# Performance work log

Measured on AMD Instinct MI355X. Metric: run time of the kernel, lower is better.

## Reference

```python
import jax, jax.numpy as jnp
import numpy as np

B, T, H, DIN, DOUT = 512, 256, 512, 514, 2
DT_OVER_TAU = 1.0 / 10.0

def retanh(a):
    return jnp.maximum(jnp.tanh(a), 0.0)

def setup_inputs() -> dict:
    key = jax.random.key(0)
    ks = jax.random.split(key, 5)
    x = jax.random.normal(ks[0], (B, T, DIN), dtype=jnp.float32)
    noise = jax.random.normal(ks[1], (B, T, H), dtype=jnp.float32) * 0.1
    W_x_ah = jax.random.normal(ks[2], (H, DIN), dtype=jnp.float32) / np.sqrt(DIN).astype(np.float32)
    b_ah = jnp.zeros((H,), dtype=jnp.float32)
    W_h_ah = jax.random.normal(ks[3], (H, H), dtype=jnp.float32) / np.sqrt(H).astype(np.float32)
    W_h_y = jnp.zeros((DOUT, H), dtype=jnp.float32)
    ah0 = jnp.zeros((H,), dtype=jnp.float32)
    return {"x": x, "noise": noise, "W_x_ah": W_x_ah, "b_ah": b_ah,
            "W_h_ah": W_h_ah, "W_h_y": W_h_y, "ah0": ah0}

def reference(x, noise, W_x_ah, b_ah, W_h_ah, W_h_y, ah0):
    batch = x.shape[0]
    # precompute input drive for all timesteps: [B,T,H]
    x2ah = jnp.einsum('btd,hd->bth', x, W_x_ah) + b_ah
    ah_init = jnp.broadcast_to(ah0, (batch, H))
    h_init = retanh(ah_init)

    def step(carry, inp):
        ah, h = carry
        xt, nt = inp  # [B,H], [B,H]
        ah = ah + DT_OVER_TAU * (-ah + h @ W_h_ah.T + xt)
        h = retanh(ah) + nt
        return (ah, h), h

    xs = (jnp.swapaxes(x2ah, 0, 1), jnp.swapaxes(noise, 0, 1))  # [T,B,H]
    _, hs = jax.lax.scan(step, (ah_init, h_init), xs)
    hstore = jnp.swapaxes(hs, 0, 1)  # [B,T,H]
    output = jnp.einsum('bth,oh->bto', hstore, W_h_y)
    return output, hstore
```

## Files before the change

### kernel.cpp

```cpp
#include <hip/hip_runtime.h>
#include <math.h>

#define BB   512
#define TT   256
#define HH   512
#define DIN  514
#define DOUTN 2
#define DT   0.1f
#define TH   (TT * HH)

#define NSL   4
#define NGRP  32

typedef short s16x8 __attribute__((ext_vector_type(8)));
typedef float f32x4 __attribute__((ext_vector_type(4)));

__device__ __forceinline__ float retanh_f(float a) {
    float am = fminf(a, 15.0f);
    float E  = __expf(2.0f * am);
    float tp = __fdividef(E - 1.0f, E + 1.0f);
    return a > 0.0f ? tp : 0.0f;
}

__device__ __forceinline__ unsigned short f2bf(float f) {
    unsigned u = __float_as_uint(f);
    unsigned r = (u + 0x7FFFu + ((u >> 16) & 1u)) >> 16;
    return (unsigned short)r;
}

__device__ __forceinline__ void gload_lds16(const void* g, void* l) {
    __builtin_amdgcn_global_load_lds(
        (const __attribute__((address_space(1))) unsigned int*)g,
        (__attribute__((address_space(3))) unsigned int*)l, 16, 0, 0);
}

__global__ __launch_bounds__(256) void pack_wh(const float* __restrict__ Wh,
                                               unsigned short* __restrict__ Wp) {
    const int idx = blockIdx.x * 256 + threadIdx.x;
    const int l  = idx & 63;
    const int jt = (idx >> 6) & 31;
    const int kc = idx >> 11;
    const int j  = jt * 16 + (l & 15);
    const int k0 = kc * 32 + (l >> 4) * 8;
    s16x8 pv;
    #pragma unroll
    for (int e = 0; e < 8; ++e) pv[e] = (short)f2bf(Wh[j * HH + k0 + e]);
    *(s16x8*)&Wp[(size_t)idx * 8] = pv;
}

__global__ __launch_bounds__(256) void pack_wx(const float* __restrict__ Wx,
                                               unsigned short* __restrict__ WfH,
                                               unsigned short* __restrict__ WfL) {
    const int idx = blockIdx.x * 256 + threadIdx.x;
    const int l  = idx & 63;
    const int jt = (idx >> 6) & 31;
    const int kc = idx >> 11;
    const int j  = jt * 16 + (l & 15);
    const int k0 = kc * 32 + (l >> 4) * 8;
    s16x8 ph, pl;
    #pragma unroll
    for (int e = 0; e < 8; ++e) {
        const float v = Wx[(size_t)j * DIN + k0 + e];
        const unsigned short hi = f2bf(v);
        const float hv = __uint_as_float((unsigned)hi << 16);
        ph[e] = (short)hi;
        pl[e] = (short)f2bf(v - hv);
    }
    *(s16x8*)&WfH[(size_t)idx * 8] = ph;
    *(s16x8*)&WfL[(size_t)idx * 8] = pl;
}

__device__ __forceinline__ void cvt_hilo(float4 a, float4 b, s16x8& hi, s16x8& lo) {
    float v[8] = {a.x, a.y, a.z, a.w, b.x, b.y, b.z, b.w};
    #pragma unroll
    for (int e = 0; e < 8; ++e) {
        const unsigned short h = f2bf(v[e]);
        hi[e] = (short)h;
        lo[e] = (short)f2bf(v[e] - __uint_as_float((unsigned)h << 16));
    }
}

#define STAGE_W(KC, DST) do { \
    const s16x8* gh = WfHv + (size_t)(KC) * 2048 + w * 256 + l; \
    const s16x8* gl = WfLv + (size_t)(KC) * 2048 + w * 256 + l; \
    s16x8* dh = (DST) + w * 256; \
    s16x8* dl = (DST) + 2048 + w * 256; \
    gload_lds16(gh + 0 * 64, dh + 0 * 64); \
    gload_lds16(gh + 1 * 64, dh + 1 * 64); \
    gload_lds16(gh + 2 * 64, dh + 2 * 64); \
    gload_lds16(gh + 3 * 64, dh + 3 * 64); \
    gload_lds16(gl + 0 * 64, dl + 0 * 64); \
    gload_lds16(gl + 1 * 64, dl + 1 * 64); \
    gload_lds16(gl + 2 * 64, dl + 2 * 64); \
    gload_lds16(gl + 3 * 64, dl + 3 * 64); \
} while (0)

__global__ __launch_bounds__(512) void x2ah_mfma(const float* __restrict__ X,
                                                 const unsigned short* __restrict__ WfH,
                                                 const unsigned short* __restrict__ WfL,
                                                 const float* __restrict__ Wx,
                                                 const float* __restrict__ bias,
                                                 const float* __restrict__ noise,
                                                 unsigned int* __restrict__ outp) {
    __shared__ __align__(16) char arena[2][65536];

    const int tid = threadIdx.x;
    const int l   = tid & 63;
    const int w   = tid >> 6;
    const int lm  = l & 15;
    const int lg  = l >> 4;
    const int lg4 = lg * 4;
    const int lg8 = lg * 8;
    const int r0  = blockIdx.x * 128;

    const int rt  = w & 3;
    const int jt0 = (w >> 2) * 16;

    const s16x8* WfHv = (const s16x8*)WfH;
    const s16x8* WfLv = (const s16x8*)WfL;

    const float* xr0 = X + (size_t)(r0 + rt * 32 + lm) * DIN;
    const float* xr1 = xr0 + 16 * DIN;

    float4 xa0 = *(const float4*)(xr0 + lg8);
    float4 xb0 = *(const float4*)(xr0 + lg8 + 4);
    float4 xa1 = *(const float4*)(xr1 + lg8);
    float4 xb1 = *(const float4*)(xr1 + lg8 + 4);
    STAGE_W(0, (s16x8*)arena[0]);
    __syncthreads();

    f32x4 acc0[16], acc1[16];
    #pragma unroll
    for (int jt = 0; jt < 16; ++jt) {
        acc0[jt] = (f32x4){0.f, 0.f, 0.f, 0.f};
        acc1[jt] = (f32x4){0.f, 0.f, 0.f, 0.f};
    }

    for (int kc = 0; kc < 16; ++kc) {
        s16x8* cur = (s16x8*)arena[kc & 1];
        s16x8* nxt = (s16x8*)arena[(kc & 1) ^ 1];
        if (kc < 15) STAGE_W(kc + 1, nxt);

        s16x8 Ah0, Al0, Ah1, Al1;
        cvt_hilo(xa0, xb0, Ah0, Al0);
        cvt_hilo(xa1, xb1, Ah1, Al1);
        if (kc < 15) {
            const int off = (kc + 1) * 32 + lg8;
            xa0 = *(const float4*)(xr0 + off);
            xb0 = *(const float4*)(xr0 + off + 4);
            xa1 = *(const float4*)(xr1 + off);
            xb1 = *(const float4*)(xr1 + off + 4);
        }

        #pragma unroll
        for (int jt = 0; jt < 16; ++jt) {
            const s16x8 Bh = cur[(jt0 + jt) * 64 + l];
            const s16x8 Bl = cur[2048 + (jt0 + jt) * 64 + l];
            acc0[jt] = __builtin_amdgcn_mfma_f32_16x16x32_bf16(Ah0, Bh, acc0[jt], 0, 0, 0);
            acc0[jt] = __builtin_amdgcn_mfma_f32_16x16x32_bf16(Al0, Bh, acc0[jt], 0, 0, 0);
            acc0[jt] = __builtin_amdgcn_mfma_f32_16x16x32_bf16(Ah0, Bl, acc0[jt], 0, 0, 0);
            acc1[jt] = __builtin_amdgcn_mfma_f32_16x16x32_bf16(Ah1, Bh, acc1[jt], 0, 0, 0);
            acc1[jt] = __builtin_amdgcn_mfma_f32_16x16x32_bf16(Al1, Bh, acc1[jt], 0, 0, 0);
            acc1[jt] = __builtin_amdgcn_mfma_f32_16x16x32_bf16(Ah1, Bl, acc1[jt], 0, 0, 0);
        }
        __syncthreads();
    }

    unsigned short* ls = (unsigned short*)arena;
    for (int c = 0; c < 8; ++c) {
        if (rt == (c >> 1)) {
            float xt0[4], xt1[4];
            #pragma unroll
            for (int r = 0; r < 4; ++r) {
                const float* xrow = X + (size_t)(r0 + c * 16 + lg4 + r) * DIN + 512;
                xt0[r] = xrow[0];
                xt1[r] = xrow[1];
            }
            #pragma unroll
            for (int jt = 0; jt < 16; ++jt) {
                const int j = (jt0 + jt) * 16 + lm;
                const float2 wt = *(const float2*)&Wx[(size_t)j * DIN + 512];
                const float bj = bias[j];
                #pragma unroll
                for (int r = 0; r < 4; ++r) {
                    const float av = (c & 1) ? acc1[jt][r] : acc0[jt][r];
                    const float v = av + bj + xt0[r] * wt.x + xt1[r] * wt.y;
                    ls[(lg4 + r) * 512 + j] = f2bf(v);
                }
            }
        }
        __syncthreads();
        {
            const int i   = tid * 16;
            const int row = i >> 9, col = i & 511;
            const size_t gi = (size_t)(r0 + c * 16 + row) * HH + col;
            const float4 n0 = *(const float4*)&noise[gi + 0];
            const float4 n1 = *(const float4*)&noise[gi + 4];
            const float4 n2 = *(const float4*)&noise[gi + 8];
            const float4 n3 = *(const float4*)&noise[gi + 12];
            const unsigned short* lp = &ls[row * 512 + col];
            const uint4 la = *(const uint4*)lp;
            const uint4 lb = *(const uint4*)(lp + 8);
            uint4 o0, o1, o2, o3;
            o0.x = ((la.x & 0xffffu) << 16) | f2bf(n0.x);
            o0.y = (la.x & 0xffff0000u)     | f2bf(n0.y);
            o0.z = ((la.y & 0xffffu) << 16) | f2bf(n0.z);
            o0.w = (la.y & 0xffff0000u)     | f2bf(n0.w);
            o1.x = ((la.z & 0xffffu) << 16) | f2bf(n1.x);
            o1.y = (la.z & 0xffff0000u)     | f2bf(n1.y);
            o1.z = ((la.w & 0xffffu) << 16) | f2bf(n1.z);
            o1.w = (la.w & 0xffff0000u)     | f2bf(n1.w);
            o2.x = ((lb.x & 0xffffu) << 16) | f2bf(n2.x);
            o2.y = (lb.x & 0xffff0000u)     | f2bf(n2.y);
            o2.z = ((lb.y & 0xffffu) << 16) | f2bf(n2.z);
            o2.w = (lb.y & 0xffff0000u)     | f2bf(n2.w);
            o3.x = ((lb.z & 0xffffu) << 16) | f2bf(n3.x);
            o3.y = (lb.z & 0xffff0000u)     | f2bf(n3.y);
            o3.z = ((lb.w & 0xffffu) << 16) | f2bf(n3.z);
            o3.w = (lb.w & 0xffff0000u)     | f2bf(n3.w);
            *(uint4*)&outp[gi + 0]  = o0;
            *(uint4*)&outp[gi + 4]  = o1;
            *(uint4*)&outp[gi + 8]  = o2;
            *(uint4*)&outp[gi + 12] = o3;
        }
        __syncthreads();
    }
}

#define WKLOAD(KC) s16x8 wk##KC = WpV[((KC) * 32 + s * 8 + w) * 64 + l]
#define WKPIN(A, B, C, D) asm volatile("" : "+v"(A), "+v"(B), "+v"(C), "+v"(D))

#define KC_EVEN(KC) do { \
    const s16x8 A = *(const s16x8*)&hrow[(KC) * 32]; \
    accA = __builtin_amdgcn_mfma_f32_16x16x32_bf16(A, wk##KC, accA, 0, 0, 0); \
} while (0)
#define KC_ODD(KC) do { \
    const s16x8 A = *(const s16x8*)&hrow[(KC) * 32]; \
    accB = __builtin_amdgcn_mfma_f32_16x16x32_bf16(A, wk##KC, accB, 0, 0, 0); \
} while (0)

__global__ __launch_bounds__(512) void scan12_kernel(const unsigned short* __restrict__ Wp,
                                                     const float* __restrict__ ah0,
                                                     unsigned int* __restrict__ hio,
                                                     unsigned short* inbox,
                                                     unsigned int* flags) {
    __shared__ __align__(16) unsigned short hs[16][520];

    const int tid = threadIdx.x;
    const int l   = tid & 63;
    const int w   = tid >> 6;
    const int lm  = l & 15;
    const int lg  = l >> 4;
    const int lg4 = lg * 4;
    const int gid = blockIdx.x;
    const int g   = gid >> 2;
    const int s   = gid & 3;
    const int b0  = g * 16;

    const s16x8* WpV = (const s16x8*)Wp;

    WKLOAD(0);  WKLOAD(1);  WKLOAD(2);  WKLOAD(3);
    WKLOAD(4);  WKLOAD(5);  WKLOAD(6);  WKLOAD(7);
    WKLOAD(8);  WKLOAD(9);  WKLOAD(10); WKLOAD(11);
    WKLOAD(12); WKLOAD(13); WKLOAD(14); WKLOAD(15);
    WKPIN(wk0, wk1, wk2, wk3);     WKPIN(wk4, wk5, wk6, wk7);
    WKPIN(wk8, wk9, wk10, wk11);   WKPIN(wk12, wk13, wk14, wk15);

    const int jn = (s * 8 + w) * 16 + lm;

    f32x4 ahv;
    {
        const float a0 = ah0[jn];
        ahv = (f32x4){a0, a0, a0, a0};
    }

    for (int idx = tid; idx < 16 * 512; idx += 512) {
        int b = idx >> 9, k = idx & 511;
        hs[b][k] = f2bf(retanh_f(ah0[k]));
    }
    __syncthreads();

    const unsigned short* hrow = &hs[lm][lg * 8];

    const int pb = tid >> 5;
    const int pq = tid & 31;
    unsigned long long* ibx = (unsigned long long*)inbox;
    const int pubIdx = (((b0 + pb) << 9) + s * 128 + pq * 4) >> 2;
    const int gatIdx = ((b0 + pb) << 7) + pq;

    int gb = (b0 + lg4) * TH + jn;

    unsigned int pk0 = hio[gb + 0 * TH];
    unsigned int pk1 = hio[gb + 1 * TH];
    unsigned int pk2 = hio[gb + 2 * TH];
    unsigned int pk3 = hio[gb + 3 * TH];

    for (int t = 0; t < TT; ++t) {
        const int par = (t & 1) << 16;

        f32x4 accA = (f32x4){0.f, 0.f, 0.f, 0.f};
        f32x4 accB = (f32x4){0.f, 0.f, 0.f, 0.f};
        KC_EVEN(0);  KC_ODD(1);  KC_EVEN(2);  KC_ODD(3);
        KC_EVEN(4);  KC_ODD(5);  KC_EVEN(6);  KC_ODD(7);
        KC_EVEN(8);  KC_ODD(9);  KC_EVEN(10); KC_ODD(11);
        KC_EVEN(12); KC_ODD(13); KC_EVEN(14); KC_ODD(15);
        const f32x4 acc = accA + accB;

        __syncthreads();

        {
            float a, h;
            unsigned int p;
            p = pk0; a = ahv[0];
            a += DT * (acc[0] + __uint_as_float(p & 0xffff0000u) - a);
            ahv[0] = a; h = retanh_f(a) + __uint_as_float(p << 16);
            hio[gb + 0 * TH] = __float_as_uint(h); hs[lg4 + 0][jn] = f2bf(h);
            p = pk1; a = ahv[1];
            a += DT * (acc[1] + __uint_as_float(p & 0xffff0000u) - a);
            ahv[1] = a; h = retanh_f(a) + __uint_as_float(p << 16);
            hio[gb + 1 * TH] = __float_as_uint(h); hs[lg4 + 1][jn] = f2bf(h);
            p = pk2; a = ahv[2];
            a += DT * (acc[2] + __uint_as_float(p & 0xffff0000u) - a);
            ahv[2] = a; h = retanh_f(a) + __uint_as_float(p << 16);
            hio[gb + 2 * TH] = __float_as_uint(h); hs[lg4 + 2][jn] = f2bf(h);
            p = pk3; a = ahv[3];
            a += DT * (acc[3] + __uint_as_float(p & 0xffff0000u) - a);
            ahv[3] = a; h = retanh_f(a) + __uint_as_float(p << 16);
            hio[gb + 3 * TH] = __float_as_uint(h); hs[lg4 + 3][jn] = f2bf(h);
        }

        __syncthreads();

        {
            const unsigned long long pub =
                *(const unsigned long long*)&hs[pb][s * 128 + pq * 4];
            __hip_atomic_store(&ibx[par + pubIdx], pub, __ATOMIC_RELAXED,
                               __HIP_MEMORY_SCOPE_AGENT);
        }
        asm volatile("s_waitcnt vmcnt(0)" ::: "memory");
        __syncthreads();

        unsigned int* fl = flags + (t * NGRP + g) * NSL;
        if (tid == 0)
            __hip_atomic_store(&fl[s], 1u, __ATOMIC_RELAXED, __HIP_MEMORY_SCOPE_AGENT);

        if (t + 1 < TT) {
            pk0 = hio[gb + HH + 0 * TH];
            pk1 = hio[gb + HH + 1 * TH];
            pk2 = hio[gb + HH + 2 * TH];
            pk3 = hio[gb + HH + 3 * TH];
        }

        if (tid < NSL) {
            while (__hip_atomic_load(&fl[tid], __ATOMIC_RELAXED,
                                     __HIP_MEMORY_SCOPE_AGENT) == 0u)
                __builtin_amdgcn_s_sleep(1);
        }
        __syncthreads();

        {
            const unsigned long long g0 = __hip_atomic_load(&ibx[par + gatIdx + 0 * 32],
                __ATOMIC_RELAXED, __HIP_MEMORY_SCOPE_AGENT);
            const unsigned long long g1 = __hip_atomic_load(&ibx[par + gatIdx + 1 * 32],
                __ATOMIC_RELAXED, __HIP_MEMORY_SCOPE_AGENT);
            const unsigned long long g2 = __hip_atomic_load(&ibx[par + gatIdx + 2 * 32],
                __ATOMIC_RELAXED, __HIP_MEMORY_SCOPE_AGENT);
            const unsigned long long g3 = __hip_atomic_load(&ibx[par + gatIdx + 3 * 32],
                __ATOMIC_RELAXED, __HIP_MEMORY_SCOPE_AGENT);
            *(unsigned long long*)&hs[pb][pq * 4 + 0 * 128] = g0;
            *(unsigned long long*)&hs[pb][pq * 4 + 1 * 128] = g1;
            *(unsigned long long*)&hs[pb][pq * 4 + 2 * 128] = g2;
            *(unsigned long long*)&hs[pb][pq * 4 + 3 * 128] = g3;
        }
        __syncthreads();

        gb += HH;
    }
}

__global__ __launch_bounds__(256) void out_kernel(const float* __restrict__ hstore,
                                                  const float* __restrict__ Wy,
                                                  float* __restrict__ out0) {
    const int wave = threadIdx.x >> 6;
    const int lane = threadIdx.x & 63;
    const int r = blockIdx.x * 4 + wave;

    const float4* hv4 = (const float4*)&hstore[r * HH];
    float a0 = 0.0f, a1 = 0.0f;
    #pragma unroll
    for (int u = 0; u < 2; ++u) {
        const int e = u * 64 + lane;
        const float4 h  = hv4[e];
        const float4 w0 = *(const float4*)&Wy[e * 4];
        const float4 w1 = *(const float4*)&Wy[HH + e * 4];
        a0 += h.x * w0.x + h.y * w0.y + h.z * w0.z + h.w * w0.w;
        a1 += h.x * w1.x + h.y * w1.y + h.z * w1.z + h.w * w1.w;
    }
    #pragma unroll
    for (int off = 32; off > 0; off >>= 1) {
        a0 += __shfl_xor(a0, off);
        a1 += __shfl_xor(a1, off);
    }
    if (lane == 0) {
        out0[r * 2]     = a0;
        out0[r * 2 + 1] = a1;
    }
}

extern "C" void kernel_launch(void* const* d_in, const int* in_sizes, int n_in,
                              void* d_out, int out_size, void* d_ws, size_t ws_size,
                              hipStream_t stream) {
    const float* x     = (const float*)d_in[0];
    const float* noise = (const float*)d_in[1];
    const float* Wx    = (const float*)d_in[2];
    const float* bah   = (const float*)d_in[3];
    const float* Wh    = (const float*)d_in[4];
    const float* Wy    = (const float*)d_in[5];
    const float* ah0   = (const float*)d_in[6];

    float* out0   = (float*)d_out;
    float* hstore = (float*)d_out + BB * TT * DOUTN;

    const size_t FRAG_U16 = (size_t)16 * 32 * 64 * 8;
    unsigned short* Wp    = (unsigned short*)d_ws;
    unsigned short* WxH   = Wp + FRAG_U16;
    unsigned short* WxL   = WxH + FRAG_U16;
    unsigned short* inbox = WxL + FRAG_U16;
    unsigned int*   flags = (unsigned int*)(inbox + 2 * BB * HH);

    pack_wh<<<16 * 32 * 64 / 256, 256, 0, stream>>>(Wh, Wp);
    pack_wx<<<16 * 32 * 64 / 256, 256, 0, stream>>>(Wx, WxH, WxL);
    x2ah_mfma<<<BB * TT / 128, 512, 0, stream>>>(x, WxH, WxL, Wx, bah, noise,
                                                 (unsigned int*)hstore);

    hipMemsetAsync(flags, 0, (size_t)TT * NGRP * NSL * sizeof(unsigned int), stream);
    {
        const unsigned short* wpp = Wp;
        unsigned int* hiop = (unsigned int*)hstore;
        unsigned short* ibp = inbox;
        unsigned int* flp = flags;
        void* args[] = { (void*)&wpp, (void*)&ah0, (void*)&hiop,
                         (void*)&ibp, (void*)&flp };
        hipLaunchCooperativeKernel((void*)scan12_kernel, dim3(NGRP * NSL),
                                   dim3(512), args, 0, stream);
    }

    out_kernel<<<BB * TT / 4, 256, 0, stream>>>(hstore, Wy, out0);
}
```

Before: 1.119 ms.

## Publish per-wave h directly to inbox with per-wave flags and fuse output projection

Each wave now writes its bf16 h values straight to the global inbox and raises its own flag, so two block-wide barriers and the shared-memory staging step before publishing are gone. Consumers spin on 32 per-wave flags instead of 4 per-block flags. The hstore writes move after the flag store, off the critical path. The separate output-projection kernel is folded into the scan using gathered bf16 h, which removes a pass over hstore but computes the output from bf16 rather than fp32 h.

New measurement: 1.192 ms. +6.5%, slower.

```diff
diff --git a/kernel.cpp b/kernel.cpp
--- a/kernel.cpp
+++ b/kernel.cpp
@@ -239,12 +239,15 @@
     accB = __builtin_amdgcn_mfma_f32_16x16x32_bf16(A, wk##KC, accB, 0, 0, 0); \
 } while (0)
 
-__global__ __launch_bounds__(512) void scan12_kernel(const unsigned short* __restrict__ Wp,
+__global__ __launch_bounds__(512) void scan15_kernel(const unsigned short* __restrict__ Wp,
                                                      const float* __restrict__ ah0,
+                                                     const float* __restrict__ Wy,
                                                      unsigned int* __restrict__ hio,
+                                                     float* __restrict__ out0,
                                                      unsigned short* inbox,
                                                      unsigned int* flags) {
     __shared__ __align__(16) unsigned short hs[16][520];
+    __shared__ float wy[2][512];
 
     const int tid = threadIdx.x;
     const int l   = tid & 63;
@@ -274,6 +277,7 @@
         ahv = (f32x4){a0, a0, a0, a0};
     }
 
+    for (int i = tid; i < 2 * 512; i += 512) wy[i >> 9][i & 511] = Wy[i];
     for (int idx = tid; idx < 16 * 512; idx += 512) {
         int b = idx >> 9, k = idx & 511;
         hs[b][k] = f2bf(retanh_f(ah0[k]));
@@ -285,8 +289,11 @@
     const int pb = tid >> 5;
     const int pq = tid & 31;
     unsigned long long* ibx = (unsigned long long*)inbox;
-    const int pubIdx = (((b0 + pb) << 9) + s * 128 + pq * 4) >> 2;
     const int gatIdx = ((b0 + pb) << 7) + pq;
+    const int pubBase = (b0 + lg4) * 512 + jn;
+
+    const int obid = 4 * s + (w >> 1);
+    const int oo   = w & 1;
 
     int gb = (b0 + lg4) * TH + jn;
 
@@ -296,7 +303,8 @@
     unsigned int pk3 = hio[gb + 3 * TH];
 
     for (int t = 0; t < TT; ++t) {
-        const int par = (t & 1) << 16;
+        const int par64 = (t & 1) << 16;
+        const int par16 = (t & 1) << 18;
 
         f32x4 accA = (f32x4){0.f, 0.f, 0.f, 0.f};
         f32x4 accB = (f32x4){0.f, 0.f, 0.f, 0.f};
@@ -306,44 +314,44 @@
         KC_EVEN(12); KC_ODD(13); KC_EVEN(14); KC_ODD(15);
         const f32x4 acc = accA + accB;
 
-        __syncthreads();
-
+        float h0f, h1f, h2f, h3f;
         {
-            float a, h;
-            unsigned int p;
-            p = pk0; a = ahv[0];
-            a += DT * (acc[0] + __uint_as_float(p & 0xffff0000u) - a);
-            ahv[0] = a; h = retanh_f(a) + __uint_as_float(p << 16);
-            hio[gb + 0 * TH] = __float_as_uint(h); hs[lg4 + 0][jn] = f2bf(h);
-            p = pk1; a = ahv[1];
-            a += DT * (acc[1] + __uint_as_float(p & 0xffff0000u) - a);
-            ahv[1] = a; h = retanh_f(a) + __uint_as_float(p << 16);
-            hio[gb + 1 * TH] = __float_as_uint(h); hs[lg4 + 1][jn] = f2bf(h);
-            p = pk2; a = ahv[2];
-            a += DT * (acc[2] + __uint_as_float(p & 0xffff0000u) - a);
-            ahv[2] = a; h = retanh_f(a) + __uint_as_float(p << 16);
-            hio[gb + 2 * TH] = __float_as_uint(h); hs[lg4 + 2][jn] = f2bf(h);
-            p = pk3; a = ahv[3];
-            a += DT * (acc[3] + __uint_as_float(p & 0xffff0000u) - a);
-            ahv[3] = a; h = retanh_f(a) + __uint_as_float(p << 16);
-            hio[gb + 3 * TH] = __float_as_uint(h); hs[lg4 + 3][jn] = f2bf(h);
-        }
-
-        __syncthreads();
+            float a;
+            a = ahv[0];
+            a += DT * (acc[0] + __uint_as_float(pk0 & 0xffff0000u) - a);
+            ahv[0] = a; h0f = retanh_f(a) + __uint_as_float(pk0 << 16);
+            a = ahv[1];
+            a += DT * (acc[1] + __uint_as_float(pk1 & 0xffff0000u) - a);
+            ahv[1] = a; h1f = retanh_f(a) + __uint_as_float(pk1 << 16);
+            a = ahv[2];
+            a += DT * (acc[2] + __uint_as_float(pk2 & 0xffff0000u) - a);
+            ahv[2] = a; h2f = retanh_f(a) + __uint_as_float(pk2 << 16);
+            a = ahv[3];
+            a += DT * (acc[3] + __uint_as_float(pk3 & 0xffff0000u) - a);
+            ahv[3] = a; h3f = retanh_f(a) + __uint_as_float(pk3 << 16);
+        }
 
         {
-            const unsigned long long pub =
-                *(const unsigned long long*)&hs[pb][s * 128 + pq * 4];
-            __hip_atomic_store(&ibx[par + pubIdx], pub, __ATOMIC_RELAXED,
+            unsigned short* pbase = inbox + par16 + pubBase;
+            __hip_atomic_store(&pbase[0 * 512], f2bf(h0f), __ATOMIC_RELAXED,
                                __HIP_MEMORY_SCOPE_AGENT);
+            __hip_atomic_store(&pbase[1 * 512], f2bf(h1f), __ATOMIC_RELAXED,
+                               __HIP_MEMORY_SCOPE_AGENT);
+            __hip_atomic_store(&pbase[2 * 512], f2bf(h2f), __ATOMIC_RELAXED,
+                               __HIP_MEMORY_SCOPE_AGENT);
+            __hip_atomic_store(&pbase[3 * 512], f2bf(h3f), __ATOMIC_RELAXED,
+                               __HIP_MEMORY_SCOPE_AGENT);
         }
         asm volatile("s_waitcnt vmcnt(0)" ::: "memory");
-        __syncthreads();
-
-        unsigned int* fl = flags + (t * NGRP + g) * NSL;
-        if (tid == 0)
-            __hip_atomic_store(&fl[s], 1u, __ATOMIC_RELAXED, __HIP_MEMORY_SCOPE_AGENT);
-
+
+        unsigned int* fl = flags + ((size_t)(t * NGRP + g) * NSL + s) * 8;
+        if (l == 0)
+            __hip_atomic_store(&fl[w], 1u, __ATOMIC_RELAXED, __HIP_MEMORY_SCOPE_AGENT);
+
+        hio[gb + 0 * TH] = __float_as_uint(h0f);
+        hio[gb + 1 * TH] = __float_as_uint(h1f);
+        hio[gb + 2 * TH] = __float_as_uint(h2f);
+        hio[gb + 3 * TH] = __float_as_uint(h3f);
         if (t + 1 < TT) {
             pk0 = hio[gb + HH + 0 * TH];
             pk1 = hio[gb + HH + 1 * TH];
@@ -351,21 +359,23 @@
             pk3 = hio[gb + HH + 3 * TH];
         }
 
-        if (tid < NSL) {
-            while (__hip_atomic_load(&fl[tid], __ATOMIC_RELAXED,
+        if (tid < 32) {
+            const unsigned int* fp = flags
+                + ((size_t)(t * NGRP + g) * NSL + (tid >> 3)) * 8 + (tid & 7);
+            while (__hip_atomic_load(fp, __ATOMIC_RELAXED,
                                      __HIP_MEMORY_SCOPE_AGENT) == 0u)
                 __builtin_amdgcn_s_sleep(1);
         }
         __syncthreads();
 
         {
-            const unsigned long long g0 = __hip_atomic_load(&ibx[par + gatIdx + 0 * 32],
+            const unsigned long long g0 = __hip_atomic_load(&ibx[par64 + gatIdx + 0 * 32],
                 __ATOMIC_RELAXED, __HIP_MEMORY_SCOPE_AGENT);
-            const unsigned long long g1 = __hip_atomic_load(&ibx[par + gatIdx + 1 * 32],
+            const unsigned long long g1 = __hip_atomic_load(&ibx[par64 + gatIdx + 1 * 32],
                 __ATOMIC_RELAXED, __HIP_MEMORY_SCOPE_AGENT);
-            const unsigned long long g2 = __hip_atomic_load(&ibx[par + gatIdx + 2 * 32],
+            const unsigned long long g2 = __hip_atomic_load(&ibx[par64 + gatIdx + 2 * 32],
                 __ATOMIC_RELAXED, __HIP_MEMORY_SCOPE_AGENT);
-            const unsigned long long g3 = __hip_atomic_load(&ibx[par + gatIdx + 3 * 32],
+            const unsigned long long g3 = __hip_atomic_load(&ibx[par64 + gatIdx + 3 * 32],
                 __ATOMIC_RELAXED, __HIP_MEMORY_SCOPE_AGENT);
             *(unsigned long long*)&hs[pb][pq * 4 + 0 * 128] = g0;
             *(unsigned long long*)&hs[pb][pq * 4 + 1 * 128] = g1;
@@ -374,36 +384,25 @@
         }
         __syncthreads();
 
+        {
+            const s16x8 hv = *(const s16x8*)&hs[obid][l * 8];
+            const float4 w0 = *(const float4*)&wy[oo][l * 8];
+            const float4 w1 = *(const float4*)&wy[oo][l * 8 + 4];
+            float p = __uint_as_float(((unsigned)(unsigned short)hv[0]) << 16) * w0.x
+                    + __uint_as_float(((unsigned)(unsigned short)hv[1]) << 16) * w0.y
+                    + __uint_as_float(((unsigned)(unsigned short)hv[2]) << 16) * w0.z
+                    + __uint_as_float(((unsigned)(unsigned short)hv[3]) << 16) * w0.w
+                    + __uint_as_float(((unsigned)(unsigned short)hv[4]) << 16) * w1.x
+                    + __uint_as_float(((unsigned)(unsigned short)hv[5]) << 16) * w1.y
+                    + __uint_as_float(((unsigned)(unsigned short)hv[6]) << 16) * w1.z
+                    + __uint_as_float(((unsigned)(unsigned short)hv[7]) << 16) * w1.w;
+            #pragma unroll
+            for (int off = 32; off > 0; off >>= 1) p += __shfl_xor(p, off);
+            if (l == 0)
+                out0[((size_t)(b0 + obid) * TT + t) * 2 + oo] = p;
+        }
+
         gb += HH;
-    }
-}
-
-__global__ __launch_bounds__(256) void out_kernel(const float* __restrict__ hstore,
-                                                  const float* __restrict__ Wy,
-                                                  float* __restrict__ out0) {
-    const int wave = threadIdx.x >> 6;
-    const int lane = threadIdx.x & 63;
-    const int r = blockIdx.x * 4 + wave;
-
-    const float4* hv4 = (const float4*)&hstore[r * HH];
-    float a0 = 0.0f, a1 = 0.0f;
-    #pragma unroll
-    for (int u = 0; u < 2; ++u) {
-        const int e = u * 64 + lane;
-        const float4 h  = hv4[e];
-        const float4 w0 = *(const float4*)&Wy[e * 4];
-        const float4 w1 = *(const float4*)&Wy[HH + e * 4];
-        a0 += h.x * w0.x + h.y * w0.y + h.z * w0.z + h.w * w0.w;
-        a1 += h.x * w1.x + h.y * w1.y + h.z * w1.z + h.w * w1.w;
-    }
-    #pragma unroll
-    for (int off = 32; off > 0; off >>= 1) {
-        a0 += __shfl_xor(a0, off);
-        a1 += __shfl_xor(a1, off);
-    }
-    if (lane == 0) {
-        out0[r * 2]     = a0;
-        out0[r * 2 + 1] = a1;
     }
 }
 
@@ -433,17 +432,17 @@
     x2ah_mfma<<<BB * TT / 128, 512, 0, stream>>>(x, WxH, WxL, Wx, bah, noise,
                                                  (unsigned int*)hstore);
 
-    hipMemsetAsync(flags, 0, (size_t)TT * NGRP * NSL * sizeof(unsigned int), stream);
+    hipMemsetAsync(flags, 0, (size_t)TT * NGRP * NSL * 8 * sizeof(unsigned int),
+                   stream);
     {
         const unsigned short* wpp = Wp;
         unsigned int* hiop = (unsigned int*)hstore;
+        float* outp = out0;
         unsigned short* ibp = inbox;
         unsigned int* flp = flags;
-        void* args[] = { (void*)&wpp, (void*)&ah0, (void*)&hiop,
-                         (void*)&ibp, (void*)&flp };
-        hipLaunchCooperativeKernel((void*)scan12_kernel, dim3(NGRP * NSL),
+        void* args[] = { (void*)&wpp, (void*)&ah0, (void*)&Wy, (void*)&hiop,
+                         (void*)&outp, (void*)&ibp, (void*)&flp };
+        hipLaunchCooperativeKernel((void*)scan15_kernel, dim3(NGRP * NSL),
                                    dim3(512), args, 0, stream);
     }
-
-    out_kernel<<<BB * TT / 4, 256, 0, stream>>>(hstore, Wy, out0);
-}
+}
```

## Interleave two batch groups per block to hide cross-block flag waits

Applied to the files above, without the earlier changes.

Each block now owns two 16-row batch groups and alternates them within a timestep. While it waits for one group's slices from the other blocks, it computes the recurrent GEMM and update for the other group, so the cross-block exchange latency overlaps useful work. The global hstore writes are also moved after the inbox publish and flag store, taking them off the critical path. The grid is halved to 64 blocks, so fewer CUs are active and each block carries twice the serial work per step.

New measurement: 1.705 ms. 1.52x slower.

```diff
diff --git a/kernel.cpp b/kernel.cpp
--- a/kernel.cpp
+++ b/kernel.cpp
@@ -230,21 +230,31 @@
 #define WKLOAD(KC) s16x8 wk##KC = WpV[((KC) * 32 + s * 8 + w) * 64 + l]
 #define WKPIN(A, B, C, D) asm volatile("" : "+v"(A), "+v"(B), "+v"(C), "+v"(D))
 
-#define KC_EVEN(KC) do { \
-    const s16x8 A = *(const s16x8*)&hrow[(KC) * 32]; \
+#define KC_EVEN(HR, KC) do { \
+    const s16x8 A = *(const s16x8*)&(HR)[(KC) * 32]; \
     accA = __builtin_amdgcn_mfma_f32_16x16x32_bf16(A, wk##KC, accA, 0, 0, 0); \
 } while (0)
-#define KC_ODD(KC) do { \
-    const s16x8 A = *(const s16x8*)&hrow[(KC) * 32]; \
+#define KC_ODD(HR, KC) do { \
+    const s16x8 A = *(const s16x8*)&(HR)[(KC) * 32]; \
     accB = __builtin_amdgcn_mfma_f32_16x16x32_bf16(A, wk##KC, accB, 0, 0, 0); \
 } while (0)
 
-__global__ __launch_bounds__(512) void scan12_kernel(const unsigned short* __restrict__ Wp,
+#define GEMM16(HR, ACC) do { \
+    f32x4 accA = (f32x4){0.f, 0.f, 0.f, 0.f}; \
+    f32x4 accB = (f32x4){0.f, 0.f, 0.f, 0.f}; \
+    KC_EVEN(HR, 0);  KC_ODD(HR, 1);  KC_EVEN(HR, 2);  KC_ODD(HR, 3); \
+    KC_EVEN(HR, 4);  KC_ODD(HR, 5);  KC_EVEN(HR, 6);  KC_ODD(HR, 7); \
+    KC_EVEN(HR, 8);  KC_ODD(HR, 9);  KC_EVEN(HR, 10); KC_ODD(HR, 11); \
+    KC_EVEN(HR, 12); KC_ODD(HR, 13); KC_EVEN(HR, 14); KC_ODD(HR, 15); \
+    ACC = accA + accB; \
+} while (0)
+
+__global__ __launch_bounds__(512) void scan16_kernel(const unsigned short* __restrict__ Wp,
                                                      const float* __restrict__ ah0,
                                                      unsigned int* __restrict__ hio,
                                                      unsigned short* inbox,
                                                      unsigned int* flags) {
-    __shared__ __align__(16) unsigned short hs[16][520];
+    __shared__ __align__(16) unsigned short hs[2][16][520];
 
     const int tid = threadIdx.x;
     const int l   = tid & 63;
@@ -253,9 +263,10 @@
     const int lg  = l >> 4;
     const int lg4 = lg * 4;
     const int gid = blockIdx.x;
-    const int g   = gid >> 2;
+    const int p   = gid >> 2;
     const int s   = gid & 3;
-    const int b0  = g * 16;
+    const int gA  = 2 * p,  gB = 2 * p + 1;
+    const int b0A = gA * 16, b0B = gB * 16;
 
     const s16x8* WpV = (const s16x8*)Wp;
 
@@ -268,113 +279,186 @@
 
     const int jn = (s * 8 + w) * 16 + lm;
 
-    f32x4 ahv;
+    f32x4 ahvA, ahvB;
     {
         const float a0 = ah0[jn];
-        ahv = (f32x4){a0, a0, a0, a0};
-    }
-
-    for (int idx = tid; idx < 16 * 512; idx += 512) {
-        int b = idx >> 9, k = idx & 511;
-        hs[b][k] = f2bf(retanh_f(ah0[k]));
+        ahvA = (f32x4){a0, a0, a0, a0};
+        ahvB = ahvA;
+    }
+
+    for (int idx = tid; idx < 2 * 16 * 512; idx += 512) {
+        int grp = idx >> 13, b = (idx >> 9) & 15, k = idx & 511;
+        hs[grp][b][k] = f2bf(retanh_f(ah0[k]));
     }
     __syncthreads();
 
-    const unsigned short* hrow = &hs[lm][lg * 8];
+    const unsigned short* hrowA = &hs[0][lm][lg * 8];
+    const unsigned short* hrowB = &hs[1][lm][lg * 8];
 
     const int pb = tid >> 5;
     const int pq = tid & 31;
     unsigned long long* ibx = (unsigned long long*)inbox;
-    const int pubIdx = (((b0 + pb) << 9) + s * 128 + pq * 4) >> 2;
-    const int gatIdx = ((b0 + pb) << 7) + pq;
-
-    int gb = (b0 + lg4) * TH + jn;
-
-    unsigned int pk0 = hio[gb + 0 * TH];
-    unsigned int pk1 = hio[gb + 1 * TH];
-    unsigned int pk2 = hio[gb + 2 * TH];
-    unsigned int pk3 = hio[gb + 3 * TH];
+    const int pubIdxA = (((b0A + pb) << 9) + s * 128 + pq * 4) >> 2;
+    const int pubIdxB = (((b0B + pb) << 9) + s * 128 + pq * 4) >> 2;
+    const int gatIdxA = ((b0A + pb) << 7) + pq;
+    const int gatIdxB = ((b0B + pb) << 7) + pq;
+
+    int gbA = (b0A + lg4) * TH + jn;
+    int gbB = (b0B + lg4) * TH + jn;
+
+    unsigned int pkA0 = hio[gbA + 0 * TH], pkA1 = hio[gbA + 1 * TH];
+    unsigned int pkA2 = hio[gbA + 2 * TH], pkA3 = hio[gbA + 3 * TH];
+    unsigned int pkB0 = hio[gbB + 0 * TH], pkB1 = hio[gbB + 1 * TH];
+    unsigned int pkB2 = hio[gbB + 2 * TH], pkB3 = hio[gbB + 3 * TH];
 
     for (int t = 0; t < TT; ++t) {
-        const int par = (t & 1) << 16;
-
-        f32x4 accA = (f32x4){0.f, 0.f, 0.f, 0.f};
-        f32x4 accB = (f32x4){0.f, 0.f, 0.f, 0.f};
-        KC_EVEN(0);  KC_ODD(1);  KC_EVEN(2);  KC_ODD(3);
-        KC_EVEN(4);  KC_ODD(5);  KC_EVEN(6);  KC_ODD(7);
-        KC_EVEN(8);  KC_ODD(9);  KC_EVEN(10); KC_ODD(11);
-        KC_EVEN(12); KC_ODD(13); KC_EVEN(14); KC_ODD(15);
-        const f32x4 acc = accA + accB;
-
-        __syncthreads();
-
+        const int parT = (t & 1) << 16;
+
+        f32x4 accAg;
+        GEMM16(hrowA, accAg);
+        __syncthreads();
+
+        float hA0, hA1, hA2, hA3;
         {
-            float a, h;
-            unsigned int p;
-            p = pk0; a = ahv[0];
-            a += DT * (acc[0] + __uint_as_float(p & 0xffff0000u) - a);
-            ahv[0] = a; h = retanh_f(a) + __uint_as_float(p << 16);
-            hio[gb + 0 * TH] = __float_as_uint(h); hs[lg4 + 0][jn] = f2bf(h);
-            p = pk1; a = ahv[1];
-            a += DT * (acc[1] + __uint_as_float(p & 0xffff0000u) - a);
-            ahv[1] = a; h = retanh_f(a) + __uint_as_float(p << 16);
-            hio[gb + 1 * TH] = __float_as_uint(h); hs[lg4 + 1][jn] = f2bf(h);
-            p = pk2; a = ahv[2];
-            a += DT * (acc[2] + __uint_as_float(p & 0xffff0000u) - a);
-            ahv[2] = a; h = retanh_f(a) + __uint_as_float(p << 16);
-            hio[gb + 2 * TH] = __float_as_uint(h); hs[lg4 + 2][jn] = f2bf(h);
-            p = pk3; a = ahv[3];
-            a += DT * (acc[3] + __uint_as_float(p & 0xffff0000u) - a);
-            ahv[3] = a; h = retanh_f(a) + __uint_as_float(p << 16);
-            hio[gb + 3 * TH] = __float_as_uint(h); hs[lg4 + 3][jn] = f2bf(h);
-        }
-
+            float a;
+            a = ahvA[0];
+            a += DT * (accAg[0] + __uint_as_float(pkA0 & 0xffff0000u) - a);
+            ahvA[0] = a; hA0 = retanh_f(a) + __uint_as_float(pkA0 << 16);
+            a = ahvA[1];
+            a += DT * (accAg[1] + __uint_as_float(pkA1 & 0xffff0000u) - a);
+            ahvA[1] = a; hA1 = retanh_f(a) + __uint_as_float(pkA1 << 16);
+            a = ahvA[2];
+            a += DT * (accAg[2] + __uint_as_float(pkA2 & 0xffff0000u) - a);
+            ahvA[2] = a; hA2 = retanh_f(a) + __uint_as_float(pkA2 << 16);
+            a = ahvA[3];
+            a += DT * (accAg[3] + __uint_as_float(pkA3 & 0xffff0000u) - a);
+            ahvA[3] = a; hA3 = retanh_f(a) + __uint_as_float(pkA3 << 16);
+            hs[0][lg4 + 0][jn] = f2bf(hA0);
+            hs[0][lg4 + 1][jn] = f2bf(hA1);
+            hs[0][lg4 + 2][jn] = f2bf(hA2);
+            hs[0][lg4 + 3][jn] = f2bf(hA3);
+        }
         __syncthreads();
 
         {
             const unsigned long long pub =
-                *(const unsigned long long*)&hs[pb][s * 128 + pq * 4];
-            __hip_atomic_store(&ibx[par + pubIdx], pub, __ATOMIC_RELAXED,
+                *(const unsigned long long*)&hs[0][pb][s * 128 + pq * 4];
+            __hip_atomic_store(&ibx[parT + pubIdxA], pub, __ATOMIC_RELAXED,
                                __HIP_MEMORY_SCOPE_AGENT);
         }
         asm volatile("s_waitcnt vmcnt(0)" ::: "memory");
-        __syncthreads();
-
-        unsigned int* fl = flags + (t * NGRP + g) * NSL;
         if (tid == 0)
-            __hip_atomic_store(&fl[s], 1u, __ATOMIC_RELAXED, __HIP_MEMORY_SCOPE_AGENT);
-
+            __hip_atomic_store(&flags[((size_t)t * NGRP + gA) * NSL + s], 1u,
+                               __ATOMIC_RELAXED, __HIP_MEMORY_SCOPE_AGENT);
+        hio[gbA + 0 * TH] = __float_as_uint(hA0);
+        hio[gbA + 1 * TH] = __float_as_uint(hA1);
+        hio[gbA + 2 * TH] = __float_as_uint(hA2);
+        hio[gbA + 3 * TH] = __float_as_uint(hA3);
         if (t + 1 < TT) {
-            pk0 = hio[gb + HH + 0 * TH];
-            pk1 = hio[gb + HH + 1 * TH];
-            pk2 = hio[gb + HH + 2 * TH];
-            pk3 = hio[gb + HH + 3 * TH];
-        }
-
-        if (tid < NSL) {
-            while (__hip_atomic_load(&fl[tid], __ATOMIC_RELAXED,
+            pkA0 = hio[gbA + HH + 0 * TH];
+            pkA1 = hio[gbA + HH + 1 * TH];
+            pkA2 = hio[gbA + HH + 2 * TH];
+            pkA3 = hio[gbA + HH + 3 * TH];
+        }
+
+        if (t > 0 && tid < NSL) {
+            const unsigned int* fp =
+                &flags[((size_t)(t - 1) * NGRP + gB) * NSL + tid];
+            while (__hip_atomic_load(fp, __ATOMIC_RELAXED,
                                      __HIP_MEMORY_SCOPE_AGENT) == 0u)
                 __builtin_amdgcn_s_sleep(1);
         }
         __syncthreads();
-
+        if (t > 0) {
+            const int parG = ((t - 1) & 1) << 16;
+            const unsigned long long g0 = __hip_atomic_load(&ibx[parG + gatIdxB + 0 * 32],
+                __ATOMIC_RELAXED, __HIP_MEMORY_SCOPE_AGENT);
+            const unsigned long long g1 = __hip_atomic_load(&ibx[parG + gatIdxB + 1 * 32],
+                __ATOMIC_RELAXED, __HIP_MEMORY_SCOPE_AGENT);
+            const unsigned long long g2 = __hip_atomic_load(&ibx[parG + gatIdxB + 2 * 32],
+                __ATOMIC_RELAXED, __HIP_MEMORY_SCOPE_AGENT);
+            const unsigned long long g3 = __hip_atomic_load(&ibx[parG + gatIdxB + 3 * 32],
+                __ATOMIC_RELAXED, __HIP_MEMORY_SCOPE_AGENT);
+            *(unsigned long long*)&hs[1][pb][pq * 4 + 0 * 128] = g0;
+            *(unsigned long long*)&hs[1][pb][pq * 4 + 1 * 128] = g1;
+            *(unsigned long long*)&hs[1][pb][pq * 4 + 2 * 128] = g2;
+            *(unsigned long long*)&hs[1][pb][pq * 4 + 3 * 128] = g3;
+        }
+        __syncthreads();
+
+        f32x4 accBg;
+        GEMM16(hrowB, accBg);
+        __syncthreads();
+
+        float hB0, hB1, hB2, hB3;
         {
-            const unsigned long long g0 = __hip_atomic_load(&ibx[par + gatIdx + 0 * 32],
-                __ATOMIC_RELAXED, __HIP_MEMORY_SCOPE_AGENT);
-            const unsigned long long g1 = __hip_atomic_load(&ibx[par + gatIdx + 1 * 32],
-                __ATOMIC_RELAXED, __HIP_MEMORY_SCOPE_AGENT);
-            const unsigned long long g2 = __hip_atomic_load(&ibx[par + gatIdx + 2 * 32],
-                __ATOMIC_RELAXED, __HIP_MEMORY_SCOPE_AGENT);
-            const unsigned long long g3 = __hip_atomic_load(&ibx[par + gatIdx + 3 * 32],
-                __ATOMIC_RELAXED, __HIP_MEMORY_SCOPE_AGENT);
-            *(unsigned long long*)&hs[pb][pq * 4 + 0 * 128] = g0;
-            *(unsigned long long*)&hs[pb][pq * 4 + 1 * 128] = g1;
-            *(unsigned long long*)&hs[pb][pq * 4 + 2 * 128] = g2;
-            *(unsigned long long*)&hs[pb][pq * 4 + 3 * 128] = g3;
-        }
-        __syncthreads();
-
-        gb += HH;
+            float a;
+            a = ahvB[0];
+            a += DT * (accBg[0] + __uint_as_float(pkB0 & 0xffff0000u) - a);
+            ahvB[0] = a; hB0 = retanh_f(a) + __uint_as_float(pkB0 << 16);
+            a = ahvB[1];
+            a += DT * (accBg[1] + __uint_as_float(pkB1 & 0xffff0000u) - a);
+            ahvB[1] = a; hB1 = retanh_f(a) + __uint_as_float(pkB1 << 16);
+            a = ahvB[2];
+            a += DT * (accBg[2] + __uint_as_float(pkB2 & 0xffff0000u) - a);
+            ahvB[2] = a; hB2 = retanh_f(a) + __uint_as_float(pkB2 << 16);
+            a = ahvB[3];
+            a += DT * (accBg[3] + __uint_as_float(pkB3 & 0xffff0000u) - a);
+            ahvB[3] = a; hB3 = retanh_f(a) + __uint_as_float(pkB3 << 16);
+            hs[1][lg4 + 0][jn] = f2bf(hB0);
+            hs[1][lg4 + 1][jn] = f2bf(hB1);
+            hs[1][lg4 + 2][jn] = f2bf(hB2);
+            hs[1][lg4 + 3][jn] = f2bf(hB3);
+        }
+        __syncthreads();
+
+        {
+            const unsigned long long pub =
+                *(const unsigned long long*)&hs[1][pb][s * 128 + pq * 4];
+            __hip_atomic_store(&ibx[parT + pubIdxB], pub, __ATOMIC_RELAXED,
+                               __HIP_MEMORY_SCOPE_AGENT);
+        }
+        asm volatile("s_waitcnt vmcnt(0)" ::: "memory");
+        if (tid == 0)
+            __hip_atomic_store(&flags[((size_t)t * NGRP + gB) * NSL + s], 1u,
+                               __ATOMIC_RELAXED, __HIP_MEMORY_SCOPE_AGENT);
+        hio[gbB + 0 * TH] = __float_as_uint(hB0);
+        hio[gbB + 1 * TH] = __float_as_uint(hB1);
+        hio[gbB + 2 * TH] = __float_as_uint(hB2);
+        hio[gbB + 3 * TH] = __float_as_uint(hB3);
+        if (t + 1 < TT) {
+            pkB0 = hio[gbB + HH + 0 * TH];
+            pkB1 = hio[gbB + HH + 1 * TH];
+            pkB2 = hio[gbB + HH + 2 * TH];
+            pkB3 = hio[gbB + HH + 3 * TH];
+        }
+
+        if (tid < NSL) {
+            const unsigned int* fp =
+                &flags[((size_t)t * NGRP + gA) * NSL + tid];
+            while (__hip_atomic_load(fp, __ATOMIC_RELAXED,
+                                     __HIP_MEMORY_SCOPE_AGENT) == 0u)
+                __builtin_amdgcn_s_sleep(1);
+        }
+        __syncthreads();
+        {
+            const unsigned long long g0 = __hip_atomic_load(&ibx[parT + gatIdxA + 0 * 32],
+                __ATOMIC_RELAXED, __HIP_MEMORY_SCOPE_AGENT);
+            const unsigned long long g1 = __hip_atomic_load(&ibx[parT + gatIdxA + 1 * 32],
+                __ATOMIC_RELAXED, __HIP_MEMORY_SCOPE_AGENT);
+            const unsigned long long g2 = __hip_atomic_load(&ibx[parT + gatIdxA + 2 * 32],
+                __ATOMIC_RELAXED, __HIP_MEMORY_SCOPE_AGENT);
+            const unsigned long long g3 = __hip_atomic_load(&ibx[parT + gatIdxA + 3 * 32],
+                __ATOMIC_RELAXED, __HIP_MEMORY_SCOPE_AGENT);
+            *(unsigned long long*)&hs[0][pb][pq * 4 + 0 * 128] = g0;
+            *(unsigned long long*)&hs[0][pb][pq * 4 + 1 * 128] = g1;
+            *(unsigned long long*)&hs[0][pb][pq * 4 + 2 * 128] = g2;
+            *(unsigned long long*)&hs[0][pb][pq * 4 + 3 * 128] = g3;
+        }
+        __syncthreads();
+
+        gbA += HH;
+        gbB += HH;
     }
 }
 
@@ -441,7 +525,7 @@
         unsigned int* flp = flags;
         void* args[] = { (void*)&wpp, (void*)&ah0, (void*)&hiop,
                          (void*)&ibp, (void*)&flp };
-        hipLaunchCooperativeKernel((void*)scan12_kernel, dim3(NGRP * NSL),
+        hipLaunchCooperativeKernel((void*)scan16_kernel, dim3(NGRP * NSL / 2),
                                    dim3(512), args, 0, stream);
     }
 
```
